# Performance work log

Hardware: AMD Instinct MI355X
Metric: run time of the kernel (lower is better)

## Reference

```python
import jax, jax.numpy as jnp
import numpy as np

HIDDEN = 2048
HEADS = 16
HEAD_DIM = HIDDEN // HEADS

def setup_inputs() -> dict:
    key = jax.random.key(0)
    ks = jax.random.split(key, 9)
    B, S = 1, 4096
    scale = 1.0 / np.sqrt(HIDDEN)
    x = jax.random.normal(ks[0], (B, S, HIDDEN), dtype=jnp.float32)
    Wq = jax.random.normal(ks[1], (HIDDEN, HIDDEN), dtype=jnp.float32) * scale
    Wk = jax.random.normal(ks[2], (HIDDEN, HIDDEN), dtype=jnp.float32) * scale
    Wv = jax.random.normal(ks[3], (HIDDEN, HIDDEN), dtype=jnp.float32) * scale
    Wo = jax.random.normal(ks[4], (HIDDEN, HIDDEN), dtype=jnp.float32) * scale
    bq = jax.random.normal(ks[5], (HIDDEN,), dtype=jnp.float32) * 0.01
    bk = jax.random.normal(ks[6], (HIDDEN,), dtype=jnp.float32) * 0.01
    bv = jax.random.normal(ks[7], (HIDDEN,), dtype=jnp.float32) * 0.01
    bo = jax.random.normal(ks[8], (HIDDEN,), dtype=jnp.float32) * 0.01
    return {"x": x, "Wq": Wq, "bq": bq, "Wk": Wk, "bk": bk, "Wv": Wv, "bv": bv, "Wo": Wo, "bo": bo}

def reference(x, Wq, bq, Wk, bk, Wv, bv, Wo, bo):
    B, S, D = x.shape
    H, Hd = HEADS, HEAD_DIM
    # projections (nn.Linear: x @ W^T + b)
    Q = (x @ Wq.T + bq).reshape(B, S, H, Hd).transpose(0, 2, 1, 3)  # [B,H,S,Hd]
    K = (x @ Wk.T + bk).reshape(B, S, H, Hd).transpose(0, 2, 1, 3)
    V = (x @ Wv.T + bv).reshape(B, S, H, Hd).transpose(0, 2, 1, 3)
    scores = jnp.einsum('bhqd,bhkd->bhqk', Q, K) / jnp.sqrt(jnp.float32(Hd))
    attn = jax.nn.softmax(scores, axis=-1)
    out = jnp.einsum('bhqk,bhkd->bhqd', attn, V)  # [B,H,S,Hd]
    out = out.transpose(0, 2, 1, 3).reshape(B, S, D)
    return out @ Wo.T + bo
```

## Files before the change

kernel.cpp:

```cpp
#include <hip/hip_runtime.h>

#define S_LEN  4096
#define DMODEL 2048
#define NHEADS 16
#define HDIM   128

typedef __bf16 bf16x8 __attribute__((ext_vector_type(8)));
typedef __bf16 bf16x2 __attribute__((ext_vector_type(2)));
typedef float  f32x4  __attribute__((ext_vector_type(4)));
typedef float  f32x16 __attribute__((ext_vector_type(16)));

__device__ __forceinline__ unsigned short f2b(float f) {
    unsigned int u = __float_as_uint(f);
    unsigned int r = (u + 0x7fffu + ((u >> 16) & 1u)) >> 16;
    return (unsigned short)r;
}

__device__ __forceinline__ unsigned int pkbf16(float a, float b) {
#if __has_builtin(__builtin_amdgcn_cvt_pk_bf16_f32)
    bf16x2 t = __builtin_amdgcn_cvt_pk_bf16_f32(a, b);
    return *(unsigned int*)&t;
#else
    return (unsigned int)f2b(a) | ((unsigned int)f2b(b) << 16);
#endif
}

__device__ __forceinline__ f32x4 mfma16(bf16x8 a, bf16x8 b, f32x4 c) {
    return __builtin_amdgcn_mfma_f32_16x16x32_bf16(a, b, c, 0, 0, 0);
}

__device__ __forceinline__ f32x16 mfma32(bf16x8 a, bf16x8 b, f32x16 c) {
    return __builtin_amdgcn_mfma_f32_32x32x16_bf16(a, b, c, 0, 0, 0);
}

__device__ __forceinline__ void ldg2lds16(const void* g, void* l) {
    __builtin_amdgcn_global_load_lds(
        (__attribute__((address_space(1))) void*)(void*)g,
        (__attribute__((address_space(3))) void*)l, 16, 0, 0);
}

__global__ __launch_bounds__(256) void cvt_bf16(
    const float* __restrict__ src, unsigned short* __restrict__ dst, int n4)
{
    int i = blockIdx.x * blockDim.x + threadIdx.x;
    if (i < n4) {
        float4 v = ((const float4*)src)[i];
        uint2 h;
        h.x = pkbf16(v.x, v.y); h.y = pkbf16(v.z, v.w);
        ((uint2*)dst)[i] = h;
    }
}

__global__ __launch_bounds__(256) void cvt_bf16_w4(
    const float* __restrict__ w0, const float* __restrict__ w1,
    const float* __restrict__ w2, const float* __restrict__ w3,
    unsigned short* __restrict__ d0, unsigned short* __restrict__ d1,
    unsigned short* __restrict__ d2, unsigned short* __restrict__ d3)
{
    const int z = blockIdx.y;
    const float* src = (z == 0) ? w0 : (z == 1) ? w1 : (z == 2) ? w2 : w3;
    unsigned short* dst = (z == 0) ? d0 : (z == 1) ? d1 : (z == 2) ? d2 : d3;
    int i = blockIdx.x * blockDim.x + threadIdx.x;
    float4 v = ((const float4*)src)[i];
    uint2 h;
    h.x = pkbf16(v.x, v.y); h.y = pkbf16(v.z, v.w);
    ((uint2*)dst)[i] = h;
}

__global__ __launch_bounds__(256, 2) void gemm_qkv(
    const unsigned short* __restrict__ xb,
    const unsigned short* __restrict__ Wqb, const float* __restrict__ bq,
    const unsigned short* __restrict__ Wkb, const float* __restrict__ bk,
    const unsigned short* __restrict__ Wvb, const float* __restrict__ bv,
    unsigned short* __restrict__ Qb, unsigned short* __restrict__ Kb,
    unsigned short* __restrict__ Vb)
{
    const int z = blockIdx.z;
    const unsigned short* B = (z == 0) ? Wqb : (z == 1) ? Wkb : Wvb;
    const float* bias        = (z == 0) ? bq  : (z == 1) ? bk  : bv;
    unsigned short* C        = (z == 0) ? Qb  : (z == 1) ? Kb  : Vb;
    const float oscale = (z == 0) ? 0.12751743f : 1.0f;

    __shared__ alignas(16) unsigned short As[128 * 32];
    __shared__ alignas(16) unsigned short Bs[128 * 32];

    const int tid = threadIdx.x;
    const int m0 = blockIdx.y * 128, n0 = blockIdx.x * 128;
    const int w = tid >> 6, lane = tid & 63, lo = lane & 15, qd = lane >> 4;
    const int wm = (w >> 1) * 64, wn = (w & 1) * 64;
    const int rsel = lane >> 2, csel = (lane & 3) * 8;

    f32x4 acc[4][4] = {};

    for (int k0 = 0; k0 < DMODEL; k0 += 32) {
#pragma unroll
        for (int i = 0; i < 2; i++) {
            int c = w * 2 + i;
            ldg2lds16(&xb[(size_t)(m0 + c * 16 + rsel) * DMODEL + k0 + csel],
                      &As[c * 512]);
            ldg2lds16(&B [(size_t)(n0 + c * 16 + rsel) * DMODEL + k0 + csel],
                      &Bs[c * 512]);
        }
        __syncthreads();

        bf16x8 af[4], bfr[4];
#pragma unroll
        for (int i = 0; i < 4; i++)
            af[i] = *(const bf16x8*)&As[(wm + i * 16 + lo) * 32 + qd * 8];
#pragma unroll
        for (int j = 0; j < 4; j++)
            bfr[j] = *(const bf16x8*)&Bs[(wn + j * 16 + lo) * 32 + qd * 8];
#pragma unroll
        for (int i = 0; i < 4; i++)
#pragma unroll
            for (int j = 0; j < 4; j++)
                acc[i][j] = mfma16(af[i], bfr[j], acc[i][j]);
        __syncthreads();
    }

#pragma unroll
    for (int j = 0; j < 4; j++) {
        int n = n0 + wn + j * 16 + lo;
        float bv_ = bias[n];
#pragma unroll
        for (int i = 0; i < 4; i++) {
#pragma unroll
            for (int r = 0; r < 4; r++) {
                int m = m0 + wm + i * 16 + qd * 4 + r;
                C[(size_t)m * DMODEL + n] = f2b((acc[i][j][r] + bv_) * oscale);
            }
        }
    }
}

__global__ __launch_bounds__(256, 2) void gemm_out(
    const unsigned short* __restrict__ Aatt, const unsigned short* __restrict__ Wob,
    const float* __restrict__ bo, float* __restrict__ out)
{
    __shared__ alignas(16) unsigned short As[128 * 32];
    __shared__ alignas(16) unsigned short Bs[128 * 32];

    const int tid = threadIdx.x;
    const int m0 = blockIdx.y * 128, n0 = blockIdx.x * 128;
    const int w = tid >> 6, lane = tid & 63, lo = lane & 15, qd = lane >> 4;
    const int wm = (w >> 1) * 64, wn = (w & 1) * 64;
    const int rsel = lane >> 2, csel = (lane & 3) * 8;

    f32x4 acc[4][4] = {};

    for (int k0 = 0; k0 < DMODEL; k0 += 32) {
#pragma unroll
        for (int i = 0; i < 2; i++) {
            int c = w * 2 + i;
            ldg2lds16(&Aatt[(size_t)(m0 + c * 16 + rsel) * DMODEL + k0 + csel],
                      &As[c * 512]);
            ldg2lds16(&Wob [(size_t)(n0 + c * 16 + rsel) * DMODEL + k0 + csel],
                      &Bs[c * 512]);
        }
        __syncthreads();

        bf16x8 af[4], bfr[4];
#pragma unroll
        for (int i = 0; i < 4; i++)
            af[i] = *(const bf16x8*)&As[(wm + i * 16 + lo) * 32 + qd * 8];
#pragma unroll
        for (int j = 0; j < 4; j++)
            bfr[j] = *(const bf16x8*)&Bs[(wn + j * 16 + lo) * 32 + qd * 8];
#pragma unroll
        for (int i = 0; i < 4; i++)
#pragma unroll
            for (int j = 0; j < 4; j++)
                acc[i][j] = mfma16(af[i], bfr[j], acc[i][j]);
        __syncthreads();
    }

#pragma unroll
    for (int j = 0; j < 4; j++) {
        int n = n0 + wn + j * 16 + lo;
        float bv_ = bo[n];
#pragma unroll
        for (int i = 0; i < 4; i++) {
#pragma unroll
            for (int r = 0; r < 4; r++) {
                int m = m0 + wm + i * 16 + qd * 4 + r;
                out[(size_t)m * DMODEL + n] = acc[i][j][r] + bv_;
            }
        }
    }
}

__global__ __launch_bounds__(256) void transpose_v(
    const unsigned short* __restrict__ Vb, unsigned short* __restrict__ Vt)
{
    __shared__ unsigned short tile[64 * 67];
    const int s0 = blockIdx.x * 64;
    const int d0 = blockIdx.y * 64;
    const int tid = threadIdx.x;
#pragma unroll
    for (int i = 0; i < 2; i++) {
        int chunk = tid + i * 256;
        int r = chunk >> 3, c8 = (chunk & 7) * 8;
        uint4 v = *(const uint4*)&Vb[(size_t)(s0 + r) * DMODEL + d0 + c8];
        const unsigned short* p = (const unsigned short*)&v;
#pragma unroll
        for (int j = 0; j < 8; j++) tile[r * 67 + c8 + j] = p[j];
    }
    __syncthreads();
#pragma unroll
    for (int i = 0; i < 2; i++) {
        int chunk = tid + i * 256;
        int r = chunk >> 3, c8 = (chunk & 7) * 8;
        unsigned short tmp[8];
#pragma unroll
        for (int j = 0; j < 8; j++) tmp[j] = tile[(c8 + j) * 67 + r];
        *(uint4*)&Vt[(size_t)(d0 + r) * S_LEN + s0 + c8] = *(uint4*)tmp;
    }
}

__global__ __launch_bounds__(256, 3) void attn_kernel(
    const unsigned short* __restrict__ Qb, const unsigned short* __restrict__ Kb,
    const unsigned short* __restrict__ Vt, unsigned short* __restrict__ Ob)
{
    const int id = blockIdx.x;
    const int xcd = id & 7, slot = id >> 3;
    const int h  = (xcd << 1) | (slot >> 6);
    const int q0 = (slot & 63) * 64;

    __shared__ alignas(16) unsigned char smem[33280];
    unsigned short* Ks  = (unsigned short*)smem;
    unsigned short* Vts = (unsigned short*)(smem + 16384);
    float* Of = (float*)smem;
    float* Lf = (float*)(smem + 32768);

    const int tid = threadIdx.x;
    const int w = tid >> 6, lane = tid & 63;
    const int qw = w >> 1, kw = w & 1;
    const int l31 = lane & 31, hi = lane >> 5;
    const int sw7 = l31 & 7;

    bf16x8 qf[8];
    {
        const unsigned short* qrow =
            &Qb[(size_t)(q0 + qw * 32 + l31) * DMODEL + h * HDIM];
#pragma unroll
        for (int sl = 0; sl < 8; sl++)
            qf[sl] = *(const bf16x8*)&qrow[sl * 16 + hi * 8];
    }

    f32x16 o_acc[4] = {};
    float l_run = 0.f;

    const int krow = kw * 32 + l31;

    for (int kb = 0; kb < S_LEN / 64; kb++) {
        const int key0 = kb * 64;

#pragma unroll
        for (int i = 0; i < 4; i++) {
            int r = w * 16 + i * 4 + (lane >> 4);
            int c = (lane & 15) ^ (r & 7);
            ldg2lds16(&Kb[(size_t)(key0 + r) * DMODEL + h * HDIM + c * 8],
                      &Ks[(w * 16 + i * 4) * 128]);
        }
#pragma unroll
        for (int i = 0; i < 4; i++) {
            int r = w * 32 + i * 8 + (lane >> 3);
            int c = (lane & 7) ^ (r & 7);
            ldg2lds16(&Vt[(size_t)(h * HDIM + r) * S_LEN + key0 + c * 8],
                      &Vts[(w * 32 + i * 8) * 64]);
        }
        __syncthreads();

        f32x16 s = {};
        __builtin_amdgcn_s_setprio(1);
#pragma unroll
        for (int sl = 0; sl < 8; sl++) {
            bf16x8 kf = *(const bf16x8*)
                &Ks[krow * 128 + (((2 * sl + hi) ^ sw7) * 8)];
            s = mfma32(kf, qf[sl], s);
        }
        __builtin_amdgcn_s_setprio(0);

        float p[16];
        {
            float ls = 0.f;
#pragma unroll
            for (int r = 0; r < 16; r++) {
                p[r] = __builtin_amdgcn_exp2f(s[r]);
                ls += p[r];
            }
            l_run += ls;
        }

        bf16x8 pa[2];
#pragma unroll
        for (int k2 = 0; k2 < 2; k2++) {
            unsigned int c0 = pkbf16(p[8 * k2 + 0], p[8 * k2 + 1]);
            unsigned int c1 = pkbf16(p[8 * k2 + 2], p[8 * k2 + 3]);
            unsigned int c2 = pkbf16(p[8 * k2 + 4], p[8 * k2 + 5]);
            unsigned int c3 = pkbf16(p[8 * k2 + 6], p[8 * k2 + 7]);
            asm("v_permlane32_swap_b32 %0, %1" : "+v"(c0), "+v"(c2));
            asm("v_permlane32_swap_b32 %0, %1" : "+v"(c1), "+v"(c3));
            uint4 u; u.x = c0; u.y = c1; u.z = c2; u.w = c3;
            pa[k2] = *(bf16x8*)&u;
        }

        __builtin_amdgcn_s_setprio(1);
#pragma unroll
        for (int k2 = 0; k2 < 2; k2++) {
            const int gch = 4 * kw + 2 * k2 + hi;
#pragma unroll
            for (int dt = 0; dt < 4; dt++) {
                bf16x8 vf = *(const bf16x8*)
                    &Vts[(dt * 32 + l31) * 64 + ((gch ^ sw7) * 8)];
                o_acc[dt] = mfma32(pa[k2], vf, o_acc[dt]);
            }
        }
        __builtin_amdgcn_s_setprio(0);

        __syncthreads();
    }

    float l = l_run + __shfl_xor(l_run, 32);

    if (kw == 1) {
#pragma unroll
        for (int dt = 0; dt < 4; dt++)
#pragma unroll
            for (int r = 0; r < 16; r++) {
                int row = (r & 3) + 8 * (r >> 2) + 4 * hi;
                Of[(qw * 32 + row) * 128 + dt * 32 + l31] = o_acc[dt][r];
            }
    }
    if (hi == 0) Lf[(qw * 2 + kw) * 32 + l31] = l;
    __syncthreads();

    if (kw == 0) {
        float linv[16];
#pragma unroll
        for (int r = 0; r < 16; r++) {
            int row = (r & 3) + 8 * (r >> 2) + 4 * hi;
            linv[r] = 1.0f / (Lf[(qw * 2 + 0) * 32 + row] +
                              Lf[(qw * 2 + 1) * 32 + row]);
        }
#pragma unroll
        for (int dt = 0; dt < 4; dt++)
#pragma unroll
            for (int r = 0; r < 16; r++) {
                int row = (r & 3) + 8 * (r >> 2) + 4 * hi;
                float v = o_acc[dt][r] + Of[(qw * 32 + row) * 128 + dt * 32 + l31];
                Ob[(size_t)(q0 + qw * 32 + row) * DMODEL + h * HDIM + dt * 32 + l31]
                    = f2b(v * linv[r]);
            }
    }
}

extern "C" void kernel_launch(void* const* d_in, const int* in_sizes, int n_in,
                              void* d_out, int out_size, void* d_ws, size_t ws_size,
                              hipStream_t stream)
{
    const float* x  = (const float*)d_in[0];
    const float* Wq = (const float*)d_in[1];
    const float* bq = (const float*)d_in[2];
    const float* Wk = (const float*)d_in[3];
    const float* bk = (const float*)d_in[4];
    const float* Wv = (const float*)d_in[5];
    const float* bv = (const float*)d_in[6];
    const float* Wo = (const float*)d_in[7];
    const float* bo = (const float*)d_in[8];
    float* out = (float*)d_out;

    const size_t N = (size_t)S_LEN * DMODEL;
    const size_t W = (size_t)DMODEL * DMODEL;
    unsigned short* Qb  = (unsigned short*)d_ws;
    unsigned short* Kb  = Qb + N;
    unsigned short* Vb  = Kb + N;
    unsigned short* xbv = Vb + N;
    unsigned short* Wqb = xbv + N;
    unsigned short* Wkb = Wqb + W;
    unsigned short* Wvb = Wkb + W;
    unsigned short* Wob = Wvb + W;
    unsigned short* Vt  = xbv;
    unsigned short* Ob  = Vb;

    cvt_bf16<<<(int)(N / 4 / 256), 256, 0, stream>>>(x, xbv, (int)(N / 4));
    cvt_bf16_w4<<<dim3((unsigned)(W / 4 / 256), 4), 256, 0, stream>>>(
        Wq, Wk, Wv, Wo, Wqb, Wkb, Wvb, Wob);

    gemm_qkv<<<dim3(DMODEL / 128, S_LEN / 128, 3), 256, 0, stream>>>(
        xbv, Wqb, bq, Wkb, bk, Wvb, bv, Qb, Kb, Vb);

    transpose_v<<<dim3(S_LEN / 64, DMODEL / 64), 256, 0, stream>>>(Vb, Vt);

    attn_kernel<<<1024, 256, 0, stream>>>(Qb, Kb, Vt, Ob);

    gemm_out<<<dim3(DMODEL / 128, S_LEN / 128), 256, 0, stream>>>(Ob, Wob, bo, out);
}
```

Baseline: 525.0 us.

## Split K/V staging to overlap loads with MFMA and raise occupancy

The K tile for the next block is now issued during the P·V MFMAs, and the V tile for the current block is issued before the Q·K MFMAs. The old load-all-then-sync pattern is replaced by a mid-iteration barrier, so global-to-LDS latency is meant to hide behind compute. The exp2, row-sum and bf16 pack steps are fused into one loop, and launch bounds go from 3 to 4 blocks per CU. The higher occupancy target tightens the register budget and may cause spills, given the 64 accumulator and 32 Q-fragment registers per lane.

```diff
diff --git a/kernel.cpp b/kernel.cpp
--- a/kernel.cpp
+++ b/kernel.cpp
@@ -217,7 +217,7 @@
     }
 }
 
-__global__ __launch_bounds__(256, 3) void attn_kernel(
+__global__ __launch_bounds__(256, 4) void attn_kernel(
     const unsigned short* __restrict__ Qb, const unsigned short* __restrict__ Kb,
     const unsigned short* __restrict__ Vt, unsigned short* __restrict__ Ob)
 {
@@ -252,24 +252,34 @@
 
     const int krow = kw * 32 + l31;
 
+#define STAGE_K(key0_)                                                        \
+    {                                                                         \
+        _Pragma("unroll")                                                     \
+        for (int i = 0; i < 4; i++) {                                         \
+            int r = w * 16 + i * 4 + (lane >> 4);                             \
+            int c = (lane & 15) ^ (r & 7);                                    \
+            ldg2lds16(&Kb[(size_t)((key0_) + r) * DMODEL + h * HDIM + c * 8], \
+                      &Ks[(w * 16 + i * 4) * 128]);                           \
+        }                                                                     \
+    }
+#define STAGE_V(key0_)                                                        \
+    {                                                                         \
+        _Pragma("unroll")                                                     \
+        for (int i = 0; i < 4; i++) {                                         \
+            int r = w * 32 + i * 8 + (lane >> 3);                             \
+            int c = (lane & 7) ^ (r & 7);                                     \
+            ldg2lds16(&Vt[(size_t)(h * HDIM + r) * S_LEN + (key0_) + c * 8],  \
+                      &Vts[(w * 32 + i * 8) * 64]);                           \
+        }                                                                     \
+    }
+
+    STAGE_K(0);
+    __syncthreads();
+
     for (int kb = 0; kb < S_LEN / 64; kb++) {
         const int key0 = kb * 64;
 
-#pragma unroll
-        for (int i = 0; i < 4; i++) {
-            int r = w * 16 + i * 4 + (lane >> 4);
-            int c = (lane & 15) ^ (r & 7);
-            ldg2lds16(&Kb[(size_t)(key0 + r) * DMODEL + h * HDIM + c * 8],
-                      &Ks[(w * 16 + i * 4) * 128]);
-        }
-#pragma unroll
-        for (int i = 0; i < 4; i++) {
-            int r = w * 32 + i * 8 + (lane >> 3);
-            int c = (lane & 7) ^ (r & 7);
-            ldg2lds16(&Vt[(size_t)(h * HDIM + r) * S_LEN + key0 + c * 8],
-                      &Vts[(w * 32 + i * 8) * 64]);
-        }
-        __syncthreads();
+        STAGE_V(key0);
 
         f32x16 s = {};
         __builtin_amdgcn_s_setprio(1);
@@ -281,45 +291,54 @@
         }
         __builtin_amdgcn_s_setprio(0);
 
-        float p[16];
+        bf16x8 pa0, pa1;
         {
             float ls = 0.f;
 #pragma unroll
-            for (int r = 0; r < 16; r++) {
-                p[r] = __builtin_amdgcn_exp2f(s[r]);
-                ls += p[r];
+            for (int k2 = 0; k2 < 2; k2++) {
+                float e0 = __builtin_amdgcn_exp2f(s[8 * k2 + 0]);
+                float e1 = __builtin_amdgcn_exp2f(s[8 * k2 + 1]);
+                float e2 = __builtin_amdgcn_exp2f(s[8 * k2 + 2]);
+                float e3 = __builtin_amdgcn_exp2f(s[8 * k2 + 3]);
+                float e4 = __builtin_amdgcn_exp2f(s[8 * k2 + 4]);
+                float e5 = __builtin_amdgcn_exp2f(s[8 * k2 + 5]);
+                float e6 = __builtin_amdgcn_exp2f(s[8 * k2 + 6]);
+                float e7 = __builtin_amdgcn_exp2f(s[8 * k2 + 7]);
+                ls += ((e0 + e1) + (e2 + e3)) + ((e4 + e5) + (e6 + e7));
+                unsigned int c0 = pkbf16(e0, e1);
+                unsigned int c1 = pkbf16(e2, e3);
+                unsigned int c2 = pkbf16(e4, e5);
+                unsigned int c3 = pkbf16(e6, e7);
+                asm("v_permlane32_swap_b32 %0, %1" : "+v"(c0), "+v"(c2));
+                asm("v_permlane32_swap_b32 %0, %1" : "+v"(c1), "+v"(c3));
+                uint4 u; u.x = c0; u.y = c1; u.z = c2; u.w = c3;
+                if (k2 == 0) pa0 = *(bf16x8*)&u; else pa1 = *(bf16x8*)&u;
             }
             l_run += ls;
         }
 
-        bf16x8 pa[2];
-#pragma unroll
-        for (int k2 = 0; k2 < 2; k2++) {
-            unsigned int c0 = pkbf16(p[8 * k2 + 0], p[8 * k2 + 1]);
-            unsigned int c1 = pkbf16(p[8 * k2 + 2], p[8 * k2 + 3]);
-            unsigned int c2 = pkbf16(p[8 * k2 + 4], p[8 * k2 + 5]);
-            unsigned int c3 = pkbf16(p[8 * k2 + 6], p[8 * k2 + 7]);
-            asm("v_permlane32_swap_b32 %0, %1" : "+v"(c0), "+v"(c2));
-            asm("v_permlane32_swap_b32 %0, %1" : "+v"(c1), "+v"(c3));
-            uint4 u; u.x = c0; u.y = c1; u.z = c2; u.w = c3;
-            pa[k2] = *(bf16x8*)&u;
-        }
+        __syncthreads();
+
+        if (kb + 1 < S_LEN / 64) STAGE_K((kb + 1) * 64);
 
         __builtin_amdgcn_s_setprio(1);
 #pragma unroll
         for (int k2 = 0; k2 < 2; k2++) {
             const int gch = 4 * kw + 2 * k2 + hi;
+            bf16x8 pf = (k2 == 0) ? pa0 : pa1;
 #pragma unroll
             for (int dt = 0; dt < 4; dt++) {
                 bf16x8 vf = *(const bf16x8*)
                     &Vts[(dt * 32 + l31) * 64 + ((gch ^ sw7) * 8)];
-                o_acc[dt] = mfma32(pa[k2], vf, o_acc[dt]);
+                o_acc[dt] = mfma32(pf, vf, o_acc[dt]);
             }
         }
         __builtin_amdgcn_s_setprio(0);
 
         __syncthreads();
     }
+#undef STAGE_K
+#undef STAGE_V
 
     float l = l_run + __shfl_xor(l_run, 32);
 
```

New measurement: 647.9 us. +23.4%, slower.
